# Performance work log

Hardware: AMD Instinct MI355X
Metric: run time of the kernel (lower is better)

Reference implementation:

```python
import jax, jax.numpy as jnp
import numpy as np

P = 7            # roi_align_size
S = 2            # sampling grid per bin (mmcv sampling_ratio fixed to 2 for static shapes)
CAV = (-140.8, -40.0, -3.0, 140.8, 40.0, 1.0)
ENLARGE = 1.0

def _bilinear(fmap, b, x, y):
    # fmap: [B,H,W,C]; b,x,y: [N,P,P,S,S]; returns [N,P,P,S,S,C]
    H, W = fmap.shape[1], fmap.shape[2]
    valid = (y > -1.0) & (y < H) & (x > -1.0) & (x < W)
    y = jnp.maximum(y, 0.0)
    x = jnp.maximum(x, 0.0)
    y0 = jnp.minimum(jnp.floor(y).astype(jnp.int32), H - 1)
    x0 = jnp.minimum(jnp.floor(x).astype(jnp.int32), W - 1)
    y1 = jnp.minimum(y0 + 1, H - 1)
    x1 = jnp.minimum(x0 + 1, W - 1)
    # mmcv: if low index is at the border, snap the coordinate onto it
    yf = jnp.where(y0 >= H - 1, y0.astype(y.dtype), y)
    xf = jnp.where(x0 >= W - 1, x0.astype(x.dtype), x)
    ly = yf - y0.astype(y.dtype); lx = xf - x0.astype(x.dtype)
    hy = 1.0 - ly; hx = 1.0 - lx
    v00 = fmap[b, y0, x0]; v01 = fmap[b, y0, x1]
    v10 = fmap[b, y1, x0]; v11 = fmap[b, y1, x1]
    out = ((hy * hx)[..., None] * v00 + (hy * lx)[..., None] * v01
           + (ly * hx)[..., None] * v10 + (ly * lx)[..., None] * v11)
    return out * valid.astype(out.dtype)[..., None]

def _forward(feature, boxes, mask):
    B, C, H, W = feature.shape
    M = boxes.shape[1]
    gw = (CAV[3] - CAV[0]) / W
    gh = (CAV[4] - CAV[1]) / H
    flat = boxes.reshape(B * M, 7)  # mask is all ones -> every box is a roi
    b_idx = jnp.repeat(jnp.arange(B, dtype=jnp.int32), M)
    # roi in grid coords; spatial_scale=1, aligned=True (center offset -0.5)
    cx = (flat[:, 0] - CAV[0]) / gw - 0.5
    cy = (flat[:, 1] - CAV[1]) / gh - 0.5
    rw = flat[:, 5] / gw * ENLARGE
    rh = flat[:, 4] / gh * ENLARGE
    theta = -flat[:, 6]             # clockwise=True -> negate angle
    bin_w = rw / P; bin_h = rh / P
    pw = jnp.arange(P, dtype=feature.dtype)
    sw = (jnp.arange(S, dtype=feature.dtype) + 0.5) / S
    # per-roi local sample coords: [N,P,S]
    xx = (-rw / 2.0)[:, None, None] + bin_w[:, None, None] * (pw[None, :, None] + sw[None, None, :])
    yy = (-rh / 2.0)[:, None, None] + bin_h[:, None, None] * (pw[None, :, None] + sw[None, None, :])
    cosv = jnp.cos(theta)[:, None, None, None, None]
    sinv = jnp.sin(theta)[:, None, None, None, None]
    Y = yy[:, :, None, :, None]     # [N,ph,1,iy,1]
    X = xx[:, None, :, None, :]     # [N,1,pw,1,ix]
    ys = Y * cosv - X * sinv + cy[:, None, None, None, None]
    xs = Y * sinv + X * cosv + cx[:, None, None, None, None]
    fmap = jnp.transpose(feature, (0, 2, 3, 1))   # [B,H,W,C] for channel-last gathers
    b = jnp.broadcast_to(b_idx[:, None, None, None, None], ys.shape)
    vals = _bilinear(fmap, b, xs, ys)             # [N,P,P,S,S,C]
    pooled = vals.mean(axis=(3, 4))               # [N,P,P,C] == torch .permute(0,2,3,1)
    return pooled

def setup_inputs():
    key = jax.random.key(0)
    k1, k2 = jax.random.split(key, 2)
    B, C, H, W, M = 4, 256, 256, 256, 100
    feature = jax.random.normal(k1, (B, C, H, W), jnp.float32)
    u = jax.random.uniform(k2, (B, M, 7), jnp.float32)
    boxes = jnp.stack([
        u[..., 0] * 200.0 - 100.0,       # x center in [-100,100] m
        u[..., 1] * 60.0 - 30.0,         # y center in [-30,30] m
        u[..., 2] * 2.0 - 1.0,           # z (unused)
        u[..., 3] * 2.0 + 1.0,           # dim (unused)
        u[..., 4] * 2.0 + 1.5,           # extent mapped to H axis
        u[..., 5] * 3.0 + 2.0,           # extent mapped to W axis
        u[..., 6] * 2.0 * np.pi - np.pi, # yaw
    ], axis=-1)
    mask = jnp.ones((B, M), jnp.float32)
    return {"feature": feature, "object_bbx_center": boxes, "object_bbx_mask": mask}

def reference(feature, object_bbx_center, object_bbx_mask):
    return _forward(feature, object_bbx_center, object_bbx_mask)
```

## Files before the change

### kernel.cpp

```cpp
#include <hip/hip_runtime.h>


#define RP 7
#define RS 2
#define RGN 16
#define CG 32
#define CSTRIDE (RGN * RGN + 1)

__global__ __launch_bounds__(256) void roialign_kernel(
    const float* __restrict__ feature,
    const float* __restrict__ boxes,
    float* __restrict__ out,
    int C, int H, int W, int M)
{
    __shared__ float sm[CG * CSTRIDE];

    const int g = blockIdx.x;
    const int n = blockIdx.y;
    const int t = threadIdx.x;
    const int b = n / M;

    const float gw = 281.6f / (float)W;
    const float gh = 80.0f  / (float)H;

    const float* bx = boxes + n * 7;
    const float cx = (bx[0] + 140.8f) / gw - 0.5f;
    const float cy = (bx[1] + 40.0f)  / gh - 0.5f;
    const float rw = bx[5] / gw;
    const float rh = bx[4] / gh;
    const float theta = -bx[6];
    const float ct = cosf(theta), st = sinf(theta);
    const float bw = rw / (float)RP, bh = rh / (float)RP;

    const float ex = 0.5f * (fabsf(rw * ct) + fabsf(rh * st));
    const float ey = 0.5f * (fabsf(rw * st) + fabsf(rh * ct));
    const int rx0 = max(0, (int)floorf(cx - ex));
    const int ry0 = max(0, (int)floorf(cy - ey));

    const int sx = t & (RGN - 1);
    const int sy = t >> 4;
    const int xg = min(rx0 + sx, W - 1);
    const int yg = min(ry0 + sy, H - 1);
    const size_t planeHW = (size_t)H * W;
    const float* fbase = feature + (size_t)(b * C + g * CG) * planeHW
                                 + (size_t)yg * W + xg;
    #pragma unroll
    for (int cs = 0; cs < CG; ++cs) {
        sm[cs * CSTRIDE + sy * RGN + sx] = fbase[(size_t)cs * planeHW];
    }
    __syncthreads();

    const int c = t & (CG - 1);
    const int slice = t >> 5;
    const float* __restrict__ smc = sm + c * CSTRIDE;
    const float Hf = (float)H, Wf = (float)W;
    float* __restrict__ outn = out + ((size_t)n * (RP * RP)) * C + g * CG + c;

    for (int bidx = slice; bidx < RP * RP; bidx += 8) {
        const int j = bidx / RP;
        const int i = bidx - j * RP;
        float acc = 0.0f;
        #pragma unroll
        for (int v = 0; v < RS; ++v) {
            const float yy = -rh * 0.5f + bh * ((float)j + ((float)v + 0.5f) / (float)RS);
            #pragma unroll
            for (int u = 0; u < RS; ++u) {
                const float xx = -rw * 0.5f + bw * ((float)i + ((float)u + 0.5f) / (float)RS);
                float y = yy * ct - xx * st + cy;
                float x = yy * st + xx * ct + cx;
                const bool valid = (y > -1.0f) & (y < Hf) & (x > -1.0f) & (x < Wf);
                y = fmaxf(y, 0.0f);
                x = fmaxf(x, 0.0f);
                const int y0 = min((int)floorf(y), H - 1);
                const int x0 = min((int)floorf(x), W - 1);
                const int y1 = min(y0 + 1, H - 1);
                const int x1 = min(x0 + 1, W - 1);
                const float ly = (y0 >= H - 1) ? 0.0f : (y - (float)y0);
                const float lx = (x0 >= W - 1) ? 0.0f : (x - (float)x0);
                const float hy = 1.0f - ly;
                const float hx = 1.0f - lx;
                const int ly0 = min(max(y0 - ry0, 0), RGN - 1);
                const int lx0 = min(max(x0 - rx0, 0), RGN - 1);
                const int ly1 = min(max(y1 - ry0, 0), RGN - 1);
                const int lx1 = min(max(x1 - rx0, 0), RGN - 1);
                const float v00 = smc[ly0 * RGN + lx0];
                const float v01 = smc[ly0 * RGN + lx1];
                const float v10 = smc[ly1 * RGN + lx0];
                const float v11 = smc[ly1 * RGN + lx1];
                const float s = hy * hx * v00 + hy * lx * v01
                              + ly * hx * v10 + ly * lx * v11;
                acc += valid ? s : 0.0f;
            }
        }
        outn[(size_t)bidx * C] = acc * (1.0f / (RS * RS));
    }
}

extern "C" void kernel_launch(void* const* d_in, const int* in_sizes, int n_in,
                              void* d_out, int out_size, void* d_ws, size_t ws_size,
                              hipStream_t stream) {
    const float* feature = (const float*)d_in[0];
    const float* boxes   = (const float*)d_in[1];
    float* out = (float*)d_out;

    const int C = 256, H = 256, W = 256;
    const int N = in_sizes[1] / 7;
    const int B = in_sizes[0] / (C * H * W);
    const int M = N / B;

    dim3 grid(C / CG, N);
    dim3 block(256);
    roialign_kernel<<<grid, block, 0, stream>>>(feature, boxes, out, C, H, W, M);
}
```

Measured before the change: 343.5 us.

## Precompute bilinear offsets/weights in LDS and load only needed ROI rows

The per-sample coordinate, index and weight maths is computed once per block by 196 threads and stored in shared memory, instead of being recomputed by every channel thread. The maximum row index actually touched is found with a shared atomicMax, and only that many rows of the 16x16 region are loaded from global memory for the 32 channels. This cuts redundant ALU work and global feature reads, at the cost of an extra barrier, an LDS atomic and more LDS traffic for reading the offsets and weights.

```diff
diff --git a/kernel.cpp b/kernel.cpp
--- a/kernel.cpp
+++ b/kernel.cpp
@@ -6,6 +6,7 @@
 #define RGN 16
 #define CG 32
 #define CSTRIDE (RGN * RGN + 1)
+#define NSAMP (RP * RP * RS * RS)
 
 __global__ __launch_bounds__(256) void roialign_kernel(
     const float* __restrict__ feature,
@@ -13,7 +14,10 @@
     float* __restrict__ out,
     int C, int H, int W, int M)
 {
-    __shared__ float sm[CG * CSTRIDE];
+    __shared__ float  sm[CG * CSTRIDE];
+    __shared__ int4   soff[NSAMP];
+    __shared__ float4 swt[NSAMP];
+    __shared__ int    srowmax;
 
     const int g = blockIdx.x;
     const int n = blockIdx.y;
@@ -34,63 +38,83 @@
 
     const float ex = 0.5f * (fabsf(rw * ct) + fabsf(rh * st));
     const float ey = 0.5f * (fabsf(rw * st) + fabsf(rh * ct));
-    const int rx0 = max(0, (int)floorf(cx - ex));
-    const int ry0 = max(0, (int)floorf(cy - ey));
+    const int rx0 = min(max(0, (int)floorf(cx - ex)), W - 1);
+    const int ry0 = min(max(0, (int)floorf(cy - ey)), H - 1);
 
+    if (t == 0) srowmax = 0;
+    __syncthreads();
+
+    const float Hf = (float)H, Wf = (float)W;
+    if (t < NSAMP) {
+        const int bin = t >> 2;
+        const int v = (t >> 1) & 1;
+        const int u = t & 1;
+        const int j = bin / RP;
+        const int i = bin - j * RP;
+        const float yy = -rh * 0.5f + bh * ((float)j + ((float)v + 0.5f) / (float)RS);
+        const float xx = -rw * 0.5f + bw * ((float)i + ((float)u + 0.5f) / (float)RS);
+        float y = yy * ct - xx * st + cy;
+        float x = yy * st + xx * ct + cx;
+        const bool valid = (y > -1.0f) & (y < Hf) & (x > -1.0f) & (x < Wf);
+        y = fmaxf(y, 0.0f);
+        x = fmaxf(x, 0.0f);
+        const int y0 = min((int)floorf(y), H - 1);
+        const int x0 = min((int)floorf(x), W - 1);
+        const int y1 = min(y0 + 1, H - 1);
+        const int x1 = min(x0 + 1, W - 1);
+        const float ly = (y0 >= H - 1) ? 0.0f : (y - (float)y0);
+        const float lx = (x0 >= W - 1) ? 0.0f : (x - (float)x0);
+        const float hy = 1.0f - ly;
+        const float hx = 1.0f - lx;
+        const int ly0 = min(max(y0 - ry0, 0), RGN - 1);
+        const int lx0 = min(max(x0 - rx0, 0), RGN - 1);
+        const int ly1 = min(max(y1 - ry0, 0), RGN - 1);
+        const int lx1 = min(max(x1 - rx0, 0), RGN - 1);
+        int4 o;
+        o.x = valid ? (ly0 * RGN + lx0) : 0;
+        o.y = valid ? (ly0 * RGN + lx1) : 0;
+        o.z = valid ? (ly1 * RGN + lx0) : 0;
+        o.w = valid ? (ly1 * RGN + lx1) : 0;
+        float4 w;
+        w.x = valid ? (hy * hx) : 0.0f;
+        w.y = valid ? (hy * lx) : 0.0f;
+        w.z = valid ? (ly * hx) : 0.0f;
+        w.w = valid ? (ly * lx) : 0.0f;
+        soff[t] = o;
+        swt[t]  = w;
+        atomicMax(&srowmax, valid ? ly1 : 0);
+    }
+    __syncthreads();
+
+    const int ny = srowmax + 1;
     const int sx = t & (RGN - 1);
     const int sy = t >> 4;
-    const int xg = min(rx0 + sx, W - 1);
-    const int yg = min(ry0 + sy, H - 1);
     const size_t planeHW = (size_t)H * W;
-    const float* fbase = feature + (size_t)(b * C + g * CG) * planeHW
-                                 + (size_t)yg * W + xg;
-    #pragma unroll
-    for (int cs = 0; cs < CG; ++cs) {
-        sm[cs * CSTRIDE + sy * RGN + sx] = fbase[(size_t)cs * planeHW];
+    if (sy < ny) {
+        const int xg = min(rx0 + sx, W - 1);
+        const int yg = min(ry0 + sy, H - 1);
+        const float* fbase = feature + (size_t)(b * C + g * CG) * planeHW
+                                     + (size_t)yg * W + xg;
+        #pragma unroll
+        for (int cs = 0; cs < CG; ++cs) {
+            sm[cs * CSTRIDE + sy * RGN + sx] = fbase[(size_t)cs * planeHW];
+        }
     }
     __syncthreads();
 
     const int c = t & (CG - 1);
     const int slice = t >> 5;
     const float* __restrict__ smc = sm + c * CSTRIDE;
-    const float Hf = (float)H, Wf = (float)W;
     float* __restrict__ outn = out + ((size_t)n * (RP * RP)) * C + g * CG + c;
 
     for (int bidx = slice; bidx < RP * RP; bidx += 8) {
-        const int j = bidx / RP;
-        const int i = bidx - j * RP;
         float acc = 0.0f;
         #pragma unroll
-        for (int v = 0; v < RS; ++v) {
-            const float yy = -rh * 0.5f + bh * ((float)j + ((float)v + 0.5f) / (float)RS);
-            #pragma unroll
-            for (int u = 0; u < RS; ++u) {
-                const float xx = -rw * 0.5f + bw * ((float)i + ((float)u + 0.5f) / (float)RS);
-                float y = yy * ct - xx * st + cy;
-                float x = yy * st + xx * ct + cx;
-                const bool valid = (y > -1.0f) & (y < Hf) & (x > -1.0f) & (x < Wf);
-                y = fmaxf(y, 0.0f);
-                x = fmaxf(x, 0.0f);
-                const int y0 = min((int)floorf(y), H - 1);
-                const int x0 = min((int)floorf(x), W - 1);
-                const int y1 = min(y0 + 1, H - 1);
-                const int x1 = min(x0 + 1, W - 1);
-                const float ly = (y0 >= H - 1) ? 0.0f : (y - (float)y0);
-                const float lx = (x0 >= W - 1) ? 0.0f : (x - (float)x0);
-                const float hy = 1.0f - ly;
-                const float hx = 1.0f - lx;
-                const int ly0 = min(max(y0 - ry0, 0), RGN - 1);
-                const int lx0 = min(max(x0 - rx0, 0), RGN - 1);
-                const int ly1 = min(max(y1 - ry0, 0), RGN - 1);
-                const int lx1 = min(max(x1 - rx0, 0), RGN - 1);
-                const float v00 = smc[ly0 * RGN + lx0];
-                const float v01 = smc[ly0 * RGN + lx1];
-                const float v10 = smc[ly1 * RGN + lx0];
-                const float v11 = smc[ly1 * RGN + lx1];
-                const float s = hy * hx * v00 + hy * lx * v01
-                              + ly * hx * v10 + ly * lx * v11;
-                acc += valid ? s : 0.0f;
-            }
+        for (int sub = 0; sub < RS * RS; ++sub) {
+            const int4   o = soff[bidx * 4 + sub];
+            const float4 w = swt[bidx * 4 + sub];
+            acc += w.x * smc[o.x] + w.y * smc[o.y]
+                 + w.z * smc[o.z] + w.w * smc[o.w];
         }
         outn[(size_t)bidx * C] = acc * (1.0f / (RS * RS));
     }
```

New measurement: 335.7 us. 1.02x faster.
